# Kernel tuning notes

Hardware: AMD Instinct MI355X
Metric: run time of the kernel (lower is better)

The kernel has to match this reference:

```python
import jax, jax.numpy as jnp
import numpy as np

HID = 1024
OUT = 512
BATCH = 512
SEQ = 128


def setup_inputs() -> dict:
    key = jax.random.key(0)
    ks = jax.random.split(key, 8)
    s = 1.0 / np.sqrt(HID)  # PyTorch LSTM/Linear init scale
    return {
        "C": jax.random.normal(ks[0], (BATCH, HID), jnp.float32),
        "t": jax.random.uniform(ks[1], (BATCH,), jnp.float32),
        "mask": jnp.ones((SEQ, BATCH), jnp.float32),
        "W_ih": jax.random.normal(ks[2], (4 * HID, HID), jnp.float32) * s,
        "W_hh": jax.random.normal(ks[3], (4 * HID, HID), jnp.float32) * s,
        "b_ih": jax.random.normal(ks[4], (4 * HID,), jnp.float32) * s,
        "b_hh": jax.random.normal(ks[5], (4 * HID,), jnp.float32) * s,
        "W_lin": jax.random.normal(ks[6], (OUT, HID), jnp.float32) * s,
        "b_lin": jax.random.normal(ks[7], (OUT,), jnp.float32) * s,
    }


def _lstm_scan(C, W_ih, W_hh, b_ih, b_hh, seq_len):
    # Input is the same C at every step -> precompute input projection once.
    x_proj = C @ W_ih.T + b_ih + b_hh  # [B, 4H]
    B, H = C.shape

    def step(carry, _):
        h, c = carry
        gates = x_proj + h @ W_hh.T  # [B, 4H]
        i, f, g, o = jnp.split(gates, 4, axis=-1)  # PyTorch gate order i,f,g,o
        i = jax.nn.sigmoid(i)
        f = jax.nn.sigmoid(f)
        g = jnp.tanh(g)
        o = jax.nn.sigmoid(o)
        c_new = f * c + i * g
        h_new = o * jnp.tanh(c_new)
        return (h_new, c_new), h_new

    h0 = jnp.zeros((B, H), C.dtype)
    c0 = jnp.zeros((B, H), C.dtype)
    _, hs = jax.lax.scan(step, (h0, c0), None, length=seq_len)
    return hs  # [T, B, H]


def reference(C, t, mask, W_ih, W_hh, b_ih, b_hh, W_lin, b_lin):
    # t and mask are unused in the original forward (t is shadowed, mask never read).
    hs = _lstm_scan(C, W_ih, W_hh, b_ih, b_hh, SEQ)  # [T, B, H]
    out = jnp.einsum("tbh,oh->tbo", hs, W_lin) + b_lin  # [T, B, O]
    return out
```

## Files before the change

kernel.cpp:

```cpp
#include <hip/hip_runtime.h>

#define B_   512
#define H_   1024
#define G4   4096
#define OUT_ 512
#define T_   128
#define APAD 72

typedef _Float16 h8  __attribute__((ext_vector_type(8)));
typedef _Float16 h4  __attribute__((ext_vector_type(4)));
typedef float    f32x4 __attribute__((ext_vector_type(4)));

#define MFMA16(a,b,c) __builtin_amdgcn_mfma_f32_16x16x32_f16(a,b,c,0,0,0)

__device__ __forceinline__ float sigmoidf_(float x) { return 1.f / (1.f + __expf(-x)); }

__global__ __launch_bounds__(256) void setup_kernel(
    const float* __restrict__ Wih, const float* __restrict__ Whh,
    const float* __restrict__ bih, const float* __restrict__ bhh,
    const float* __restrict__ Wlin,
    _Float16* __restrict__ Wih16, _Float16* __restrict__ Whh16,
    _Float16* __restrict__ Wlin16, float* __restrict__ bsum,
    float* __restrict__ cblob, _Float16* __restrict__ h0) {
  int i = blockIdx.x * blockDim.x + threadIdx.x;
  int stride = gridDim.x * blockDim.x;
  const f32x4* wih4 = (const f32x4*)Wih;
  const f32x4* whh4 = (const f32x4*)Whh;
  h4* wih16 = (h4*)Wih16;
  h4* whh16 = (h4*)Whh16;
  f32x4 z = {};
  for (int idx = i; idx < (G4 * H_) / 4; idx += stride) {
    f32x4 a = wih4[idx], b = whh4[idx];
    h4 va, vb;
#pragma unroll
    for (int r = 0; r < 4; ++r) { va[r] = (_Float16)a[r]; vb[r] = (_Float16)b[r]; }
    wih16[idx] = va; whh16[idx] = vb;
    if (idx < (OUT_ * H_) / 4) {
      f32x4 c = ((const f32x4*)Wlin)[idx];
      h4 vc;
#pragma unroll
      for (int r = 0; r < 4; ++r) vc[r] = (_Float16)c[r];
      ((h4*)Wlin16)[idx] = vc;
      ((f32x4*)cblob)[idx] = z;
    }
    if (idx < (B_ * H_ * 2) / 16)
      ((f32x4*)h0)[idx] = z;
    if (idx < G4 / 4)
      ((f32x4*)bsum)[idx] = ((const f32x4*)bih)[idx] + ((const f32x4*)bhh)[idx];
  }
}

__device__ __forceinline__ void proj_tile(int pid,
                                          const _Float16* __restrict__ h,
                                          const _Float16* __restrict__ Wlin16,
                                          const float* __restrict__ blin,
                                          float* __restrict__ outp,
                                          _Float16* smem) {
  int m0 = (pid >> 3) * 32, n0 = (pid & 7) * 64;
  int tid = threadIdx.x, w = tid >> 6, lane = tid & 63;
  _Float16* A_s = smem;
  _Float16* B_s = smem + 32 * APAD;
  f32x4 acc[2] = {};
  int fr_row = lane & 15, fr_k = (lane >> 4) * 8;
  int ar = tid >> 3, ac = (tid & 7) * 8;
  int br = tid >> 2, bq = (tid & 3) * 16;

  for (int kt = 0; kt < 16; ++kt) {
    int k0 = kt * 64;
    *(h8*)&A_s[ar * APAD + ac] = *(const h8*)(h + (size_t)(m0 + ar) * H_ + k0 + ac);
    const _Float16* bsrc = Wlin16 + (size_t)(n0 + br) * H_ + k0 + bq;
    *(h8*)&B_s[br * APAD + bq]     = *(const h8*)bsrc;
    *(h8*)&B_s[br * APAD + bq + 8] = *(const h8*)(bsrc + 8);
    __syncthreads();
#pragma unroll
    for (int s2 = 0; s2 < 2; ++s2) {
      int ks = s2 * 32 + fr_k;
      h8 a0 = *(const h8*)&A_s[fr_row * APAD + ks];
      h8 a1 = *(const h8*)&A_s[(16 + fr_row) * APAD + ks];
      h8 b  = *(const h8*)&B_s[(w * 16 + fr_row) * APAD + ks];
      acc[0] = MFMA16(a0, b, acc[0]);
      acc[1] = MFMA16(a1, b, acc[1]);
    }
    __syncthreads();
  }
  float* fr = (float*)smem + w * 512;
  float bl = blin[n0 + w * 16 + fr_row];
#pragma unroll
  for (int mf = 0; mf < 2; ++mf)
#pragma unroll
    for (int r = 0; r < 4; ++r)
      fr[((lane >> 4) * 4 + r + mf * 16) * 16 + fr_row] = acc[mf][r] + bl;
  __syncthreads();
  int row = lane >> 2, q = (lane & 3) * 4;
#pragma unroll
  for (int p = 0; p < 2; ++p) {
    f32x4 v = *(f32x4*)&fr[(row + p * 16) * 16 + q];
    *(f32x4*)(outp + (size_t)(m0 + row + p * 16) * OUT_ + n0 + w * 16 + q) = v;
  }
}

template <int IS_XPROJ>
__global__ __launch_bounds__(256) void gates_step_kernel(
    const void* __restrict__ Ag, const _Float16* __restrict__ Wg,
    const float* __restrict__ bsum, float* __restrict__ xblob,
    float* __restrict__ cblob, _Float16* __restrict__ hout,
    const _Float16* __restrict__ Wlin16, const float* __restrict__ blin,
    float* __restrict__ outp) {
  __shared__ __align__(16) _Float16 smem[64 * APAD + 128 * APAD];

  if (!IS_XPROJ && blockIdx.x >= 256) {
    proj_tile(blockIdx.x - 256, (const _Float16*)Ag, Wlin16, blin, outp, smem);
    return;
  }

  int blk = blockIdx.x;
  int xcd = blk & 7, kq = blk >> 3;
  int j_idx = xcd * 4 + (kq & 3), m_idx = kq >> 2;
  int m0 = m_idx * 64, j0 = j_idx * 32;
  int tid = threadIdx.x, w = tid >> 6, lane = tid & 63;
  int mhalf = w >> 1, jhalf = w & 1;
  _Float16* A_s = smem;
  _Float16* B_s = smem + 64 * APAD;
  f32x4 acc[4][2] = {};
  int fr_row = lane & 15, fr_k = (lane >> 4) * 8;
  int ar = tid >> 2, ac = (tid & 3) * 16;
  int r128 = tid >> 1, bg = r128 >> 5, brr = r128 & 31, bh = (tid & 1) * 32;
  const _Float16* Brow = Wg + (size_t)(bg * H_ + j0 + brr) * H_ + bh;

  for (int kt = 0; kt < 16; ++kt) {
    int k0 = kt * 64;
    if (IS_XPROJ) {
      const float* Af = (const float*)Ag;
      const f32x4* p = (const f32x4*)(Af + (size_t)(m0 + ar) * H_ + k0 + ac);
      f32x4 v0 = p[0], v1 = p[1], v2 = p[2], v3 = p[3];
      h8 hv0, hv1;
#pragma unroll
      for (int r = 0; r < 4; ++r) {
        hv0[r] = (_Float16)v0[r]; hv0[4 + r] = (_Float16)v1[r];
        hv1[r] = (_Float16)v2[r]; hv1[4 + r] = (_Float16)v3[r];
      }
      *(h8*)&A_s[ar * APAD + ac] = hv0;
      *(h8*)&A_s[ar * APAD + ac + 8] = hv1;
    } else {
      const _Float16* Ah = (const _Float16*)Ag;
      const h8* p = (const h8*)(Ah + (size_t)(m0 + ar) * H_ + k0 + ac);
      *(h8*)&A_s[ar * APAD + ac] = p[0];
      *(h8*)&A_s[ar * APAD + ac + 8] = p[1];
    }
    {
      const h8* src = (const h8*)(Brow + k0);
      _Float16* dst = &B_s[(bg * 32 + brr) * APAD + bh];
#pragma unroll
      for (int q = 0; q < 4; ++q) *(h8*)&dst[q * 8] = src[q];
    }
    __syncthreads();
#pragma unroll
    for (int s2 = 0; s2 < 2; ++s2) {
      int ks = s2 * 32 + fr_k;
      h8 a0 = *(const h8*)&A_s[(mhalf * 32 + fr_row) * APAD + ks];
      h8 a1 = *(const h8*)&A_s[(mhalf * 32 + 16 + fr_row) * APAD + ks];
#pragma unroll
      for (int g = 0; g < 4; ++g) {
        h8 b = *(const h8*)&B_s[(g * 32 + jhalf * 16 + fr_row) * APAD + ks];
        acc[g][0] = MFMA16(a0, b, acc[g][0]);
        acc[g][1] = MFMA16(a1, b, acc[g][1]);
      }
    }
    __syncthreads();
  }

  if (IS_XPROJ) {
    f32x4* xb = (f32x4*)xblob;
#pragma unroll
    for (int g = 0; g < 4; ++g) {
      float bs = bsum[g * H_ + j0 + jhalf * 16 + fr_row];
#pragma unroll
      for (int mf = 0; mf < 2; ++mf) {
        f32x4 v = acc[g][mf];
        v += bs;
        xb[(size_t)(blk * 32 + w * 8 + g * 2 + mf) * 64 + lane] = v;
      }
    }
  } else {
    f32x4* xb = (f32x4*)xblob;
    f32x4* cb = (f32x4*)cblob;
    _Float16* hr = smem + w * 512;
#pragma unroll
    for (int mf = 0; mf < 2; ++mf) {
      f32x4 xi = xb[(size_t)(blk * 32 + w * 8 + 0 + mf) * 64 + lane];
      f32x4 xf = xb[(size_t)(blk * 32 + w * 8 + 2 + mf) * 64 + lane];
      f32x4 xg = xb[(size_t)(blk * 32 + w * 8 + 4 + mf) * 64 + lane];
      f32x4 xo = xb[(size_t)(blk * 32 + w * 8 + 6 + mf) * 64 + lane];
      f32x4 cv = cb[(size_t)(blk * 8 + w * 2 + mf) * 64 + lane];
      f32x4 cn, hn;
#pragma unroll
      for (int r = 0; r < 4; ++r) {
        float iv = sigmoidf_(acc[0][mf][r] + xi[r]);
        float fv = sigmoidf_(acc[1][mf][r] + xf[r]);
        float gv = tanhf(acc[2][mf][r] + xg[r]);
        float ov = sigmoidf_(acc[3][mf][r] + xo[r]);
        float cc = fv * cv[r] + iv * gv;
        cn[r] = cc;
        hn[r] = ov * tanhf(cc);
      }
      cb[(size_t)(blk * 8 + w * 2 + mf) * 64 + lane] = cn;
#pragma unroll
      for (int r = 0; r < 4; ++r)
        hr[((lane >> 4) * 4 + r + mf * 16) * 16 + fr_row] = (_Float16)hn[r];
    }
    __syncthreads();
    int row = lane >> 1, hb2 = (lane & 1) * 8;
    h8 hv = *(const h8*)&hr[row * 16 + hb2];
    *(h8*)(hout + (size_t)(m0 + mhalf * 32 + row) * H_ + j0 + jhalf * 16 + hb2) = hv;
  }
}

__global__ __launch_bounds__(256) void proj_kernel(const _Float16* __restrict__ h,
                                                   const _Float16* __restrict__ Wlin16,
                                                   const float* __restrict__ blin,
                                                   float* __restrict__ outp) {
  __shared__ __align__(16) _Float16 smem[64 * APAD + 128 * APAD];
  proj_tile(blockIdx.x, h, Wlin16, blin, outp, smem);
}

extern "C" void kernel_launch(void* const* d_in, const int* in_sizes, int n_in,
                              void* d_out, int out_size, void* d_ws, size_t ws_size,
                              hipStream_t stream) {
  const float* C    = (const float*)d_in[0];
  const float* Wih  = (const float*)d_in[3];
  const float* Whh  = (const float*)d_in[4];
  const float* bih  = (const float*)d_in[5];
  const float* bhh  = (const float*)d_in[6];
  const float* Wlin = (const float*)d_in[7];
  const float* blin = (const float*)d_in[8];
  float* out = (float*)d_out;

  char* ws = (char*)d_ws;
  size_t off = 0;
  auto alloc = [&](size_t bytes) {
    void* p = ws + off;
    off = (off + bytes + 255) & ~(size_t)255;
    return p;
  };
  _Float16* Wih16  = (_Float16*)alloc((size_t)G4 * H_ * 2);
  _Float16* Whh16  = (_Float16*)alloc((size_t)G4 * H_ * 2);
  _Float16* Wlin16 = (_Float16*)alloc((size_t)OUT_ * H_ * 2);
  float*    bsum   = (float*)alloc((size_t)G4 * 4);
  float*    xblob  = (float*)alloc((size_t)B_ * G4 * 4);
  float*    cblob  = (float*)alloc((size_t)B_ * H_ * 4);
  _Float16* hb0    = (_Float16*)alloc((size_t)B_ * H_ * 2);
  _Float16* hb1    = (_Float16*)alloc((size_t)B_ * H_ * 2);
  if (off > ws_size) return;

  hipLaunchKernelGGL(setup_kernel, dim3(4096), dim3(256), 0, stream,
                     Wih, Whh, bih, bhh, Wlin, Wih16, Whh16, Wlin16, bsum, cblob, hb0);

  hipLaunchKernelGGL((gates_step_kernel<1>), dim3(256), dim3(256), 0, stream,
                     (const void*)C, Wih16, bsum, xblob, (float*)nullptr,
                     (_Float16*)nullptr, (const _Float16*)nullptr,
                     (const float*)nullptr, (float*)nullptr);

  _Float16* hb[2] = {hb0, hb1};
  for (int s = 1; s <= T_; ++s) {
    const _Float16* hin = hb[(s - 1) & 1];
    _Float16* ho = hb[s & 1];
    int grid = (s >= 2) ? 384 : 256;
    float* outp = (s >= 2) ? (out + (size_t)(s - 2) * B_ * OUT_) : out;
    hipLaunchKernelGGL((gates_step_kernel<0>), dim3(grid), dim3(256), 0, stream,
                       (const void*)hin, Whh16, bsum, xblob, cblob, ho, Wlin16, blin, outp);
  }
  hipLaunchKernelGGL(proj_kernel, dim3(128), dim3(256), 0, stream,
                     hb[0], Wlin16, blin, out + (size_t)(T_ - 1) * B_ * OUT_);
}
```

Before: 2.533 ms.

## Double-buffer LDS in gate GEMM and batch output projection into one kernel

Result: no change. 2.541 ms (+0.3%).

```diff
diff --git a/kernel.cpp b/kernel.cpp
--- a/kernel.cpp
+++ b/kernel.cpp
@@ -6,6 +6,7 @@
 #define OUT_ 512
 #define T_   128
 #define APAD 72
+#define BUFH (192 * APAD)
 
 typedef _Float16 h8  __attribute__((ext_vector_type(8)));
 typedef _Float16 h4  __attribute__((ext_vector_type(4)));
@@ -106,7 +107,7 @@
     float* __restrict__ cblob, _Float16* __restrict__ hout,
     const _Float16* __restrict__ Wlin16, const float* __restrict__ blin,
     float* __restrict__ outp) {
-  __shared__ __align__(16) _Float16 smem[64 * APAD + 128 * APAD];
+  __shared__ __align__(16) _Float16 smem[2 * BUFH];
 
   if (!IS_XPROJ && blockIdx.x >= 256) {
     proj_tile(blockIdx.x - 256, (const _Float16*)Ag, Wlin16, blin, outp, smem);
@@ -119,57 +120,95 @@
   int m0 = m_idx * 64, j0 = j_idx * 32;
   int tid = threadIdx.x, w = tid >> 6, lane = tid & 63;
   int mhalf = w >> 1, jhalf = w & 1;
-  _Float16* A_s = smem;
-  _Float16* B_s = smem + 64 * APAD;
   f32x4 acc[4][2] = {};
   int fr_row = lane & 15, fr_k = (lane >> 4) * 8;
   int ar = tid >> 2, ac = (tid & 3) * 16;
   int r128 = tid >> 1, bg = r128 >> 5, brr = r128 & 31, bh = (tid & 1) * 32;
   const _Float16* Brow = Wg + (size_t)(bg * H_ + j0 + brr) * H_ + bh;
-
+  const _Float16* Ah = (const _Float16*)Ag;
+  const float*    Af = (const float*)Ag;
+
+  f32x4 px[8], pc[2];
+  if constexpr (!IS_XPROJ) {
+    const f32x4* xb = (const f32x4*)xblob;
+    const f32x4* cb = (const f32x4*)cblob;
+#pragma unroll
+    for (int g = 0; g < 4; ++g)
+#pragma unroll
+      for (int mf = 0; mf < 2; ++mf)
+        px[g * 2 + mf] = xb[(size_t)(blk * 32 + w * 8 + g * 2 + mf) * 64 + lane];
+    pc[0] = cb[(size_t)(blk * 8 + w * 2 + 0) * 64 + lane];
+    pc[1] = cb[(size_t)(blk * 8 + w * 2 + 1) * 64 + lane];
+  }
+
+  h8 ra0, ra1, rb0, rb1, rb2, rb3;
+  f32x4 rv0, rv1, rv2, rv3;
+
+#define LOADK(K0) do {                                                        \
+    if constexpr (IS_XPROJ) {                                                 \
+      const f32x4* p_ = (const f32x4*)(Af + (size_t)(m0 + ar) * H_ + (K0) + ac); \
+      rv0 = p_[0]; rv1 = p_[1]; rv2 = p_[2]; rv3 = p_[3];                     \
+    } else {                                                                  \
+      const h8* p_ = (const h8*)(Ah + (size_t)(m0 + ar) * H_ + (K0) + ac);    \
+      ra0 = p_[0]; ra1 = p_[1];                                               \
+    }                                                                         \
+    const h8* bs_ = (const h8*)(Brow + (K0));                                 \
+    rb0 = bs_[0]; rb1 = bs_[1]; rb2 = bs_[2]; rb3 = bs_[3];                   \
+  } while (0)
+
+#define STOREK(BUF) do {                                                      \
+    _Float16* As_ = smem + (BUF) * BUFH;                                      \
+    _Float16* Bs_ = As_ + 64 * APAD;                                          \
+    if constexpr (IS_XPROJ) {                                                 \
+      h8 hv0, hv1;                                                            \
+      _Pragma("unroll")                                                       \
+      for (int r_ = 0; r_ < 4; ++r_) {                                        \
+        hv0[r_] = (_Float16)rv0[r_]; hv0[4 + r_] = (_Float16)rv1[r_];         \
+        hv1[r_] = (_Float16)rv2[r_]; hv1[4 + r_] = (_Float16)rv3[r_];         \
+      }                                                                       \
+      *(h8*)&As_[ar * APAD + ac] = hv0;                                       \
+      *(h8*)&As_[ar * APAD + ac + 8] = hv1;                                   \
+    } else {                                                                  \
+      *(h8*)&As_[ar * APAD + ac] = ra0;                                       \
+      *(h8*)&As_[ar * APAD + ac + 8] = ra1;                                   \
+    }                                                                         \
+    _Float16* dst_ = &Bs_[(bg * 32 + brr) * APAD + bh];                       \
+    *(h8*)&dst_[0] = rb0; *(h8*)&dst_[8] = rb1;                               \
+    *(h8*)&dst_[16] = rb2; *(h8*)&dst_[24] = rb3;                             \
+  } while (0)
+
+#define COMPUTEK(BUF) do {                                                    \
+    const _Float16* As_ = smem + (BUF) * BUFH;                                \
+    const _Float16* Bs_ = As_ + 64 * APAD;                                    \
+    _Pragma("unroll")                                                         \
+    for (int s2 = 0; s2 < 2; ++s2) {                                          \
+      int ks = s2 * 32 + fr_k;                                                \
+      h8 a0 = *(const h8*)&As_[(mhalf * 32 + fr_row) * APAD + ks];            \
+      h8 a1 = *(const h8*)&As_[(mhalf * 32 + 16 + fr_row) * APAD + ks];       \
+      _Pragma("unroll")                                                       \
+      for (int g = 0; g < 4; ++g) {                                           \
+        h8 b = *(const h8*)&Bs_[(g * 32 + jhalf * 16 + fr_row) * APAD + ks];  \
+        acc[g][0] = MFMA16(a0, b, acc[g][0]);                                 \
+        acc[g][1] = MFMA16(a1, b, acc[g][1]);                                 \
+      }                                                                       \
+    }                                                                         \
+  } while (0)
+
+  LOADK(0);
+  STOREK(0);
+  __syncthreads();
+#pragma unroll
   for (int kt = 0; kt < 16; ++kt) {
-    int k0 = kt * 64;
-    if (IS_XPROJ) {
-      const float* Af = (const float*)Ag;
-      const f32x4* p = (const f32x4*)(Af + (size_t)(m0 + ar) * H_ + k0 + ac);
-      f32x4 v0 = p[0], v1 = p[1], v2 = p[2], v3 = p[3];
-      h8 hv0, hv1;
-#pragma unroll
-      for (int r = 0; r < 4; ++r) {
-        hv0[r] = (_Float16)v0[r]; hv0[4 + r] = (_Float16)v1[r];
-        hv1[r] = (_Float16)v2[r]; hv1[4 + r] = (_Float16)v3[r];
-      }
-      *(h8*)&A_s[ar * APAD + ac] = hv0;
-      *(h8*)&A_s[ar * APAD + ac + 8] = hv1;
-    } else {
-      const _Float16* Ah = (const _Float16*)Ag;
-      const h8* p = (const h8*)(Ah + (size_t)(m0 + ar) * H_ + k0 + ac);
-      *(h8*)&A_s[ar * APAD + ac] = p[0];
-      *(h8*)&A_s[ar * APAD + ac + 8] = p[1];
-    }
-    {
-      const h8* src = (const h8*)(Brow + k0);
-      _Float16* dst = &B_s[(bg * 32 + brr) * APAD + bh];
-#pragma unroll
-      for (int q = 0; q < 4; ++q) *(h8*)&dst[q * 8] = src[q];
-    }
+    if (kt < 15) LOADK((kt + 1) * 64);
+    COMPUTEK(kt & 1);
+    if (kt < 15) STOREK((kt + 1) & 1);
     __syncthreads();
-#pragma unroll
-    for (int s2 = 0; s2 < 2; ++s2) {
-      int ks = s2 * 32 + fr_k;
-      h8 a0 = *(const h8*)&A_s[(mhalf * 32 + fr_row) * APAD + ks];
-      h8 a1 = *(const h8*)&A_s[(mhalf * 32 + 16 + fr_row) * APAD + ks];
-#pragma unroll
-      for (int g = 0; g < 4; ++g) {
-        h8 b = *(const h8*)&B_s[(g * 32 + jhalf * 16 + fr_row) * APAD + ks];
-        acc[g][0] = MFMA16(a0, b, acc[g][0]);
-        acc[g][1] = MFMA16(a1, b, acc[g][1]);
-      }
-    }
-    __syncthreads();
-  }
-
-  if (IS_XPROJ) {
+  }
+#undef LOADK
+#undef STOREK
+#undef COMPUTEK
+
+  if constexpr (IS_XPROJ) {
     f32x4* xb = (f32x4*)xblob;
 #pragma unroll
     for (int g = 0; g < 4; ++g) {
@@ -182,24 +221,18 @@
       }
     }
   } else {
-    f32x4* xb = (f32x4*)xblob;
     f32x4* cb = (f32x4*)cblob;
     _Float16* hr = smem + w * 512;
 #pragma unroll
     for (int mf = 0; mf < 2; ++mf) {
-      f32x4 xi = xb[(size_t)(blk * 32 + w * 8 + 0 + mf) * 64 + lane];
-      f32x4 xf = xb[(size_t)(blk * 32 + w * 8 + 2 + mf) * 64 + lane];
-      f32x4 xg = xb[(size_t)(blk * 32 + w * 8 + 4 + mf) * 64 + lane];
-      f32x4 xo = xb[(size_t)(blk * 32 + w * 8 + 6 + mf) * 64 + lane];
-      f32x4 cv = cb[(size_t)(blk * 8 + w * 2 + mf) * 64 + lane];
       f32x4 cn, hn;
 #pragma unroll
       for (int r = 0; r < 4; ++r) {
-        float iv = sigmoidf_(acc[0][mf][r] + xi[r]);
-        float fv = sigmoidf_(acc[1][mf][r] + xf[r]);
-        float gv = tanhf(acc[2][mf][r] + xg[r]);
-        float ov = sigmoidf_(acc[3][mf][r] + xo[r]);
-        float cc = fv * cv[r] + iv * gv;
+        float iv = sigmoidf_(acc[0][mf][r] + px[0 + mf][r]);
+        float fv = sigmoidf_(acc[1][mf][r] + px[2 + mf][r]);
+        float gv = tanhf(acc[2][mf][r] + px[4 + mf][r]);
+        float ov = sigmoidf_(acc[3][mf][r] + px[6 + mf][r]);
+        float cc = fv * pc[mf][r] + iv * gv;
         cn[r] = cc;
         hn[r] = ov * tanhf(cc);
       }
@@ -215,11 +248,95 @@
   }
 }
 
+__global__ __launch_bounds__(256) void proj_big_kernel(
+    const _Float16* __restrict__ h,
+    const _Float16* __restrict__ Wlin16, const float* __restrict__ blin,
+    float* __restrict__ outp) {
+  __shared__ __align__(16) _Float16 smem[2 * BUFH];
+  int pid = blockIdx.x;
+  int n0 = (pid & 3) * 128;
+  size_t m0 = (size_t)(pid >> 2) * 64;
+  int tid = threadIdx.x, w = tid >> 6, lane = tid & 63;
+  int fr_row = lane & 15, fr_k = (lane >> 4) * 8;
+  int ar = tid >> 2, ac = (tid & 3) * 16;
+  int br = tid >> 1, bq = (tid & 1) * 32;
+  const _Float16* Arow = h + (m0 + ar) * H_ + ac;
+  const _Float16* Brow = Wlin16 + (size_t)(n0 + br) * H_ + bq;
+  f32x4 acc[4][2] = {};
+  h8 ra0, ra1, rb0, rb1, rb2, rb3;
+
+#define LOADP(K0) do {                                                        \
+    const h8* pa_ = (const h8*)(Arow + (K0));                                 \
+    ra0 = pa_[0]; ra1 = pa_[1];                                               \
+    const h8* pb_ = (const h8*)(Brow + (K0));                                 \
+    rb0 = pb_[0]; rb1 = pb_[1]; rb2 = pb_[2]; rb3 = pb_[3];                   \
+  } while (0)
+
+#define STOREP(BUF) do {                                                      \
+    _Float16* As_ = smem + (BUF) * BUFH;                                      \
+    _Float16* Bs_ = As_ + 64 * APAD;                                          \
+    *(h8*)&As_[ar * APAD + ac] = ra0;                                         \
+    *(h8*)&As_[ar * APAD + ac + 8] = ra1;                                     \
+    _Float16* dst_ = &Bs_[br * APAD + bq];                                    \
+    *(h8*)&dst_[0] = rb0; *(h8*)&dst_[8] = rb1;                               \
+    *(h8*)&dst_[16] = rb2; *(h8*)&dst_[24] = rb3;                             \
+  } while (0)
+
+#define COMPUTEP(BUF) do {                                                    \
+    const _Float16* As_ = smem + (BUF) * BUFH;                                \
+    const _Float16* Bs_ = As_ + 64 * APAD;                                    \
+    _Pragma("unroll")                                                         \
+    for (int s2 = 0; s2 < 2; ++s2) {                                          \
+      int ks = s2 * 32 + fr_k;                                                \
+      h8 b0 = *(const h8*)&Bs_[(w * 32 + fr_row) * APAD + ks];                \
+      h8 b1 = *(const h8*)&Bs_[(w * 32 + 16 + fr_row) * APAD + ks];           \
+      _Pragma("unroll")                                                       \
+      for (int mf = 0; mf < 4; ++mf) {                                        \
+        h8 a = *(const h8*)&As_[(mf * 16 + fr_row) * APAD + ks];              \
+        acc[mf][0] = MFMA16(a, b0, acc[mf][0]);                               \
+        acc[mf][1] = MFMA16(a, b1, acc[mf][1]);                               \
+      }                                                                       \
+    }                                                                         \
+  } while (0)
+
+  LOADP(0);
+  STOREP(0);
+  __syncthreads();
+#pragma unroll
+  for (int kt = 0; kt < 16; ++kt) {
+    if (kt < 15) LOADP((kt + 1) * 64);
+    COMPUTEP(kt & 1);
+    if (kt < 15) STOREP((kt + 1) & 1);
+    __syncthreads();
+  }
+#undef LOADP
+#undef STOREP
+#undef COMPUTEP
+
+  float* fr = (float*)smem + w * 2048;
+  float bl0 = blin[n0 + w * 32 + fr_row];
+  float bl1 = blin[n0 + w * 32 + 16 + fr_row];
+#pragma unroll
+  for (int mf = 0; mf < 4; ++mf)
+#pragma unroll
+    for (int r = 0; r < 4; ++r) {
+      fr[(mf * 16 + (lane >> 4) * 4 + r) * 32 + fr_row]      = acc[mf][0][r] + bl0;
+      fr[(mf * 16 + (lane >> 4) * 4 + r) * 32 + 16 + fr_row] = acc[mf][1][r] + bl1;
+    }
+  __syncthreads();
+#pragma unroll
+  for (int p = 0; p < 8; ++p) {
+    int row = p * 8 + (lane >> 3), q = (lane & 7) * 4;
+    f32x4 v = *(f32x4*)&fr[row * 32 + q];
+    *(f32x4*)(outp + (m0 + row) * OUT_ + n0 + w * 32 + q) = v;
+  }
+}
+
 __global__ __launch_bounds__(256) void proj_kernel(const _Float16* __restrict__ h,
                                                    const _Float16* __restrict__ Wlin16,
                                                    const float* __restrict__ blin,
                                                    float* __restrict__ outp) {
-  __shared__ __align__(16) _Float16 smem[64 * APAD + 128 * APAD];
+  __shared__ __align__(16) _Float16 smem[2 * BUFH];
   proj_tile(blockIdx.x, h, Wlin16, blin, outp, smem);
 }
 
@@ -248,27 +365,50 @@
   float*    bsum   = (float*)alloc((size_t)G4 * 4);
   float*    xblob  = (float*)alloc((size_t)B_ * G4 * 4);
   float*    cblob  = (float*)alloc((size_t)B_ * H_ * 4);
-  _Float16* hb0    = (_Float16*)alloc((size_t)B_ * H_ * 2);
-  _Float16* hb1    = (_Float16*)alloc((size_t)B_ * H_ * 2);
-  if (off > ws_size) return;
-
-  hipLaunchKernelGGL(setup_kernel, dim3(4096), dim3(256), 0, stream,
-                     Wih, Whh, bih, bhh, Wlin, Wih16, Whh16, Wlin16, bsum, cblob, hb0);
-
-  hipLaunchKernelGGL((gates_step_kernel<1>), dim3(256), dim3(256), 0, stream,
-                     (const void*)C, Wih16, bsum, xblob, (float*)nullptr,
-                     (_Float16*)nullptr, (const _Float16*)nullptr,
-                     (const float*)nullptr, (float*)nullptr);
-
-  _Float16* hb[2] = {hb0, hb1};
-  for (int s = 1; s <= T_; ++s) {
-    const _Float16* hin = hb[(s - 1) & 1];
-    _Float16* ho = hb[s & 1];
-    int grid = (s >= 2) ? 384 : 256;
-    float* outp = (s >= 2) ? (out + (size_t)(s - 2) * B_ * OUT_) : out;
-    hipLaunchKernelGGL((gates_step_kernel<0>), dim3(grid), dim3(256), 0, stream,
-                       (const void*)hin, Whh16, bsum, xblob, cblob, ho, Wlin16, blin, outp);
-  }
-  hipLaunchKernelGGL(proj_kernel, dim3(128), dim3(256), 0, stream,
-                     hb[0], Wlin16, blin, out + (size_t)(T_ - 1) * B_ * OUT_);
-}
+
+  const size_t BH = (size_t)B_ * H_;
+  size_t hist_need = off + (size_t)(T_ + 1) * BH * 2;
+  bool hist = hist_need <= ws_size;
+
+  if (hist) {
+    _Float16* hs = (_Float16*)alloc((size_t)(T_ + 1) * BH * 2);
+
+    hipLaunchKernelGGL(setup_kernel, dim3(4096), dim3(256), 0, stream,
+                       Wih, Whh, bih, bhh, Wlin, Wih16, Whh16, Wlin16, bsum,
+                       cblob, hs );
+    hipLaunchKernelGGL((gates_step_kernel<1>), dim3(256), dim3(256), 0, stream,
+                       (const void*)C, Wih16, bsum, xblob, (float*)nullptr,
+                       (_Float16*)nullptr, Wlin16, blin, (float*)nullptr);
+    for (int s = 1; s <= T_; ++s) {
+      hipLaunchKernelGGL((gates_step_kernel<0>), dim3(256), dim3(256), 0, stream,
+                         (const void*)(hs + (size_t)(s - 1) * BH), Whh16, bsum,
+                         xblob, cblob, hs + (size_t)s * BH, Wlin16, blin,
+                         (float*)nullptr);
+    }
+    hipLaunchKernelGGL(proj_big_kernel, dim3((T_ * B_ / 64) * (OUT_ / 128)),
+                       dim3(256), 0, stream, hs + BH, Wlin16, blin, out);
+  } else {
+    _Float16* hb0 = (_Float16*)alloc(BH * 2);
+    _Float16* hb1 = (_Float16*)alloc(BH * 2);
+    if (off > ws_size) return;
+
+    hipLaunchKernelGGL(setup_kernel, dim3(4096), dim3(256), 0, stream,
+                       Wih, Whh, bih, bhh, Wlin, Wih16, Whh16, Wlin16, bsum,
+                       cblob, hb0);
+    hipLaunchKernelGGL((gates_step_kernel<1>), dim3(256), dim3(256), 0, stream,
+                       (const void*)C, Wih16, bsum, xblob, (float*)nullptr,
+                       (_Float16*)nullptr, Wlin16, blin, (float*)nullptr);
+    _Float16* hb[2] = {hb0, hb1};
+    for (int s = 1; s <= T_; ++s) {
+      const _Float16* hin = hb[(s - 1) & 1];
+      _Float16* ho = hb[s & 1];
+      int grid = (s >= 2) ? 384 : 256;
+      float* outp = (s >= 2) ? (out + (size_t)(s - 2) * B_ * OUT_) : out;
+      hipLaunchKernelGGL((gates_step_kernel<0>), dim3(grid), dim3(256), 0, stream,
+                         (const void*)hin, Whh16, bsum, xblob, cblob, ho,
+                         Wlin16, blin, outp);
+    }
+    hipLaunchKernelGGL(proj_kernel, dim3(128), dim3(256), 0, stream,
+                       hb[0], Wlin16, blin, out + (size_t)(T_ - 1) * B_ * OUT_);
+  }
+}
```
